# Optimization experiments

Measured on AMD Instinct MI355X. Metric: run time of the kernel, lower is better.

## Reference

```python
import jax, jax.numpy as jnp
import numpy as np

N_SRC = 50000
N_DST = 50000
N_EDGE = 600000
HID = 128
NUM_R = 6  # num_ratings + 1 weight matrices


def setup_inputs() -> dict:
    key = jax.random.key(0)
    ks = jax.random.split(key, 8)
    return {
        "src_features": jax.random.normal(ks[0], (N_SRC, HID), dtype=jnp.float32),
        "dst_features": jax.random.normal(ks[1], (N_DST, HID), dtype=jnp.float32),
        "W_r": jax.random.normal(ks[2], (NUM_R, HID, HID), dtype=jnp.float32),
        "W_lin": jax.random.normal(ks[3], (HID, 2 * HID), dtype=jnp.float32) / np.sqrt(2.0 * HID),
        "b_lin": jax.random.normal(ks[4], (HID,), dtype=jnp.float32) * 0.01,
        "edge_src": jax.random.randint(ks[5], (N_EDGE,), 0, N_SRC, dtype=jnp.int32),
        "edge_dst": jax.random.randint(ks[6], (N_EDGE,), 0, N_DST, dtype=jnp.int32),
        "rating": jax.random.randint(ks[7], (N_EDGE,), 0, NUM_R, dtype=jnp.int32),
    }


def reference(src_features, dst_features, W_r, W_lin, b_lin, edge_src, edge_dst, rating):
    # Gather source features per edge: [E, H]
    h_src = src_features[edge_src]
    # Per-edge rating-indexed matvec m_e = W_r[rating_e] @ h_src_e.
    # Avoid materializing [E, H, H] gathered weights: loop over the small
    # fixed set of rating matrices and mask-accumulate dense GEMMs.
    num_r = W_r.shape[0]
    m = jnp.zeros_like(h_src)
    for r in range(num_r):
        m = m + jnp.where((rating == r)[:, None], h_src @ W_r[r].T, jnp.zeros((), h_src.dtype))
    # Mean aggregation into destination nodes (0 for isolated nodes, like DGL).
    num_dst = dst_features.shape[0]
    sums = jax.ops.segment_sum(m, edge_dst, num_segments=num_dst)
    counts = jax.ops.segment_sum(jnp.ones((m.shape[0],), m.dtype), edge_dst, num_segments=num_dst)
    h_neigh = sums / jnp.maximum(counts, 1.0)[:, None]
    # concat + linear + relu
    h_cat = jnp.concatenate([dst_features, h_neigh], axis=1)  # [N_dst, 2H]
    return jax.nn.relu(h_cat @ W_lin.T + b_lin)
```

## Files before the change

### kernel.cpp

```cpp
#include <hip/hip_runtime.h>

#define HID 128
#define BM 128
#define BN 128
#define BKS 32
#define ALD 36
#define SCAN_BLK 256
#define SCAN_ELEMS 1024

typedef float v4f __attribute__((ext_vector_type(4)));
typedef short v4s __attribute__((ext_vector_type(4)));
typedef short v8s __attribute__((ext_vector_type(8)));

__device__ __forceinline__ void split_bf16(float v, unsigned short& hi, unsigned short& lo) {
  const unsigned int u = __float_as_uint(v);
  hi = (unsigned short)(u >> 16);
  const float rem = v - __uint_as_float(u & 0xffff0000u);
  lo = (unsigned short)(__float_as_uint(rem) >> 16);
}

__global__ void compose_Bt(const float* __restrict__ W_lin, const float* __restrict__ W_r,
                           unsigned short* __restrict__ Bth, unsigned short* __restrict__ Btl,
                           int KT) {
  const int k = blockIdx.x;
  const int n = threadIdx.x;
  float v;
  if (k < HID) {
    v = W_lin[n * (2 * HID) + k];
  } else {
    const int rr = (k - HID) >> 7;
    const int j  = (k - HID) & (HID - 1);
    const float* wl = W_lin + n * (2 * HID) + HID;
    const float* wr = W_r + (size_t)rr * HID * HID + j;
    float acc = 0.f;
#pragma unroll 8
    for (int i2 = 0; i2 < HID; ++i2)
      acc = fmaf(wl[i2], wr[i2 * HID], acc);
    v = acc;
  }
  unsigned short hi, lo;
  split_bf16(v, hi, lo);
  Bth[(size_t)n * KT + k] = hi;
  Btl[(size_t)n * KT + k] = lo;
}

__global__ void hist_kernel(const int* __restrict__ ed, const int* __restrict__ er,
                            int* __restrict__ hist, int NE, int NUMR) {
  const int i = blockIdx.x * blockDim.x + threadIdx.x;
  if (i < NE) atomicAdd(hist + ed[i] * NUMR + er[i], 1);
}

__global__ __launch_bounds__(SCAN_BLK)
void scan_phaseA(const int* __restrict__ cnt, int* __restrict__ partials, int n) {
  __shared__ int red[SCAN_BLK];
  const int tid = threadIdx.x;
  const int base = blockIdx.x * SCAN_ELEMS + tid * 4;
  int s = 0;
#pragma unroll
  for (int j = 0; j < 4; ++j) {
    const int i = base + j;
    if (i < n) s += cnt[i];
  }
  red[tid] = s;
  __syncthreads();
  for (int off = SCAN_BLK / 2; off > 0; off >>= 1) {
    if (tid < off) red[tid] += red[tid + off];
    __syncthreads();
  }
  if (tid == 0) partials[blockIdx.x] = red[0];
}

__global__ __launch_bounds__(1024)
void scan_phaseB(int* __restrict__ partials, int* __restrict__ offs_n, int nb) {
  __shared__ int ps[1024];
  const int tid = threadIdx.x;
  const int chunk = (nb + 1023) / 1024;
  const int b0 = tid * chunk;
  const int e0 = min(b0 + chunk, nb);
  int s = 0;
  for (int i = b0; i < e0; ++i) s += partials[i];
  ps[tid] = s;
  __syncthreads();
  for (int off = 1; off < 1024; off <<= 1) {
    const int t = (tid >= off) ? ps[tid - off] : 0;
    __syncthreads();
    ps[tid] += t;
    __syncthreads();
  }
  int run = ps[tid] - s;
  for (int i = b0; i < e0; ++i) {
    const int c = partials[i];
    partials[i] = run;
    run += c;
  }
  if (tid == 1023) offs_n[0] = ps[1023];
}

__global__ __launch_bounds__(SCAN_BLK)
void scan_phaseC(const int* __restrict__ cnt, const int* __restrict__ partials,
                 int* __restrict__ offs, int* __restrict__ cursor, int n) {
  __shared__ int tsum[SCAN_BLK];
  const int tid = threadIdx.x;
  const int base = blockIdx.x * SCAN_ELEMS + tid * 4;
  int v[4];
  int s = 0;
#pragma unroll
  for (int j = 0; j < 4; ++j) {
    const int i = base + j;
    v[j] = (i < n) ? cnt[i] : 0;
    s += v[j];
  }
  tsum[tid] = s;
  __syncthreads();
  for (int off = 1; off < SCAN_BLK; off <<= 1) {
    const int t = (tid >= off) ? tsum[tid - off] : 0;
    __syncthreads();
    tsum[tid] += t;
    __syncthreads();
  }
  int run = partials[blockIdx.x] + tsum[tid] - s;
#pragma unroll
  for (int j = 0; j < 4; ++j) {
    const int i = base + j;
    if (i < n) {
      offs[i] = run;
      cursor[i] = run;
      run += v[j];
    }
  }
}

__global__ void reorder_kernel(const int* __restrict__ es, const int* __restrict__ ed,
                               const int* __restrict__ er, int* __restrict__ cursor,
                               int* __restrict__ sorted, int NE, int NUMR) {
  const int i = blockIdx.x * blockDim.x + threadIdx.x;
  if (i < NE) {
    const int key = ed[i] * NUMR + er[i];
    const int pos = atomicAdd(cursor + key, 1);
    sorted[pos] = es[i];
  }
}

template <int NR>
__global__ __launch_bounds__(256)
void aggregate_dst(const float* __restrict__ src, const int* __restrict__ sorted,
                   const int* __restrict__ offs, float* __restrict__ S, int NDST) {
  const int d = (blockIdx.x * (blockDim.x >> 6)) + (threadIdx.x >> 6);
  if (d >= NDST) return;
  const int lane = threadIdx.x & 63;
  const int half = lane >> 5;
  const int c4 = (lane & 31) * 4;

  const int base = d * NR;
  const int o0 = offs[base];
  const int oN = offs[base + NR];
  int bnd[NR - 1];
#pragma unroll
  for (int r = 0; r < NR - 1; ++r) bnd[r] = offs[base + 1 + r];
  const float inv = 1.0f / fmaxf((float)(oN - o0), 1.0f);

  v4f a[NR];
#pragma unroll
  for (int r = 0; r < NR; ++r) a[r] = (v4f){0.f, 0.f, 0.f, 0.f};

  for (int e = o0 + half; e < oN; e += 2) {
    const int s = sorted[e];
    const v4f v = *reinterpret_cast<const v4f*>(src + (size_t)s * HID + c4);
    int rloc = 0;
#pragma unroll
    for (int r = 0; r < NR - 1; ++r) rloc += (e >= bnd[r]) ? 1 : 0;
#pragma unroll
    for (int r = 0; r < NR; ++r) {
      if (rloc == r) a[r] += v;
    }
  }

#pragma unroll
  for (int r = 0; r < NR; ++r) {
    v4f t = a[r];
    v4f o;
    o[0] = __shfl_xor(t[0], 32);
    o[1] = __shfl_xor(t[1], 32);
    o[2] = __shfl_xor(t[2], 32);
    o[3] = __shfl_xor(t[3], 32);
    t += o;
    if (half == 0) {
      t *= inv;
      __builtin_nontemporal_store(t,
          reinterpret_cast<v4f*>(S + (size_t)d * (NR * HID) + r * HID + c4));
    }
  }
}

__global__ __launch_bounds__(256)
void aggregate_kernel(const float* __restrict__ src, const int* __restrict__ sorted,
                      const int* __restrict__ offs, float* __restrict__ S,
                      int NDST, int NUMR) {
  const int wid = (blockIdx.x * (blockDim.x >> 6)) + (threadIdx.x >> 6);
  const int lane = threadIdx.x & 63;
  if (wid >= NDST * NUMR) return;
  const int d = wid / NUMR;
  const int rloc = wid - d * NUMR;
  const int k = d * NUMR + rloc;
  const int o0 = offs[k], o1 = offs[k + 1];
  const int c0 = offs[d * NUMR], c1 = offs[d * NUMR + NUMR];
  const float inv = 1.0f / fmaxf((float)(c1 - c0), 1.0f);
  float ax = 0.f, ay = 0.f;
  for (int e = o0; e < o1; ++e) {
    const int s = sorted[e];
    const float2 v = *reinterpret_cast<const float2*>(src + (size_t)s * HID + lane * 2);
    ax += v.x; ay += v.y;
  }
  *reinterpret_cast<float2*>(S + (size_t)d * (NUMR * HID) + rloc * HID + lane * 2) =
      make_float2(ax * inv, ay * inv);
}

__global__ __launch_bounds__(512)
void mfma_gemm(const float* __restrict__ dstf, const float* __restrict__ S,
               const unsigned short* __restrict__ Bth, const unsigned short* __restrict__ Btl,
               const float* __restrict__ b_lin, float* __restrict__ out,
               int M, int KT) {
  __shared__ unsigned short Ah[2][BM][ALD], Al[2][BM][ALD];
  __shared__ unsigned short Bh[2][BN][ALD], Bl[2][BN][ALD];

  const int tid = threadIdx.x;
  const int lane = tid & 63;
  const int wid = tid >> 6;
  const int wm = wid >> 1;
  const int wn = wid & 1;
  const int m0 = blockIdx.x * BM;
  const int l15 = lane & 15;
  const int kq = (lane >> 4) * 8;

  const int arow = tid >> 2;
  const int ac8 = (tid & 3) * 8;
  const int argr = m0 + arow;
  const int SSTRIDE = KT - HID;
  const int nkt = KT / BKS;

  v4f acc[2][4];
#pragma unroll
  for (int i = 0; i < 2; ++i)
#pragma unroll
    for (int j = 0; j < 4; ++j) acc[i][j] = (v4f){0.f, 0.f, 0.f, 0.f};

  float aReg[8];
  v8s bhReg, blReg;

  auto loadTile = [&](int kg) {
    v4f v0 = (v4f){0.f, 0.f, 0.f, 0.f};
    v4f v1 = (v4f){0.f, 0.f, 0.f, 0.f};
    if (argr < M) {
      const float* p = (kg < HID)
          ? dstf + (size_t)argr * HID + kg + ac8
          : S + (size_t)argr * SSTRIDE + (kg - HID) + ac8;
      v0 = __builtin_nontemporal_load(reinterpret_cast<const v4f*>(p));
      v1 = __builtin_nontemporal_load(reinterpret_cast<const v4f*>(p + 4));
    }
    aReg[0] = v0[0]; aReg[1] = v0[1]; aReg[2] = v0[2]; aReg[3] = v0[3];
    aReg[4] = v1[0]; aReg[5] = v1[1]; aReg[6] = v1[2]; aReg[7] = v1[3];
    const size_t gb = (size_t)arow * KT + kg + ac8;
    bhReg = *reinterpret_cast<const v8s*>(Bth + gb);
    blReg = *reinterpret_cast<const v8s*>(Btl + gb);
  };

  auto writeTile = [&](int p) {
    union { v4s v[2]; unsigned short u[8]; } hh, ll;
#pragma unroll
    for (int j = 0; j < 8; ++j) split_bf16(aReg[j], hh.u[j], ll.u[j]);
    *reinterpret_cast<v4s*>(&Ah[p][arow][ac8])     = hh.v[0];
    *reinterpret_cast<v4s*>(&Ah[p][arow][ac8 + 4]) = hh.v[1];
    *reinterpret_cast<v4s*>(&Al[p][arow][ac8])     = ll.v[0];
    *reinterpret_cast<v4s*>(&Al[p][arow][ac8 + 4]) = ll.v[1];
    union { v8s v; v4s h[2]; } bu;
    bu.v = bhReg;
    *reinterpret_cast<v4s*>(&Bh[p][arow][ac8])     = bu.h[0];
    *reinterpret_cast<v4s*>(&Bh[p][arow][ac8 + 4]) = bu.h[1];
    bu.v = blReg;
    *reinterpret_cast<v4s*>(&Bl[p][arow][ac8])     = bu.h[0];
    *reinterpret_cast<v4s*>(&Bl[p][arow][ac8 + 4]) = bu.h[1];
  };

  loadTile(0);
  writeTile(0);
  __syncthreads();

  int p = 0;
  for (int kt = 0; kt < nkt; ++kt) {
    const bool hasNext = (kt + 1) < nkt;
    if (hasNext) loadTile((kt + 1) * BKS);

    union { v8s v; v4s h[2]; } afh[2], afl[2], bfh[4], bfl[4];
#pragma unroll
    for (int fm = 0; fm < 2; ++fm) {
      const int r = wm * 32 + fm * 16 + l15;
      afh[fm].h[0] = *reinterpret_cast<const v4s*>(&Ah[p][r][kq]);
      afh[fm].h[1] = *reinterpret_cast<const v4s*>(&Ah[p][r][kq + 4]);
      afl[fm].h[0] = *reinterpret_cast<const v4s*>(&Al[p][r][kq]);
      afl[fm].h[1] = *reinterpret_cast<const v4s*>(&Al[p][r][kq + 4]);
    }
#pragma unroll
    for (int fn = 0; fn < 4; ++fn) {
      const int c = wn * 64 + fn * 16 + l15;
      bfh[fn].h[0] = *reinterpret_cast<const v4s*>(&Bh[p][c][kq]);
      bfh[fn].h[1] = *reinterpret_cast<const v4s*>(&Bh[p][c][kq + 4]);
      bfl[fn].h[0] = *reinterpret_cast<const v4s*>(&Bl[p][c][kq]);
      bfl[fn].h[1] = *reinterpret_cast<const v4s*>(&Bl[p][c][kq + 4]);
    }
#pragma unroll
    for (int fm = 0; fm < 2; ++fm)
#pragma unroll
      for (int fn = 0; fn < 4; ++fn) {
        acc[fm][fn] = __builtin_amdgcn_mfma_f32_16x16x32_bf16(afh[fm].v, bfh[fn].v, acc[fm][fn], 0, 0, 0);
        acc[fm][fn] = __builtin_amdgcn_mfma_f32_16x16x32_bf16(afh[fm].v, bfl[fn].v, acc[fm][fn], 0, 0, 0);
        acc[fm][fn] = __builtin_amdgcn_mfma_f32_16x16x32_bf16(afl[fm].v, bfh[fn].v, acc[fm][fn], 0, 0, 0);
      }

    if (hasNext) writeTile(p ^ 1);
    __syncthreads();
    p ^= 1;
  }

#pragma unroll
  for (int fn = 0; fn < 4; ++fn) {
    const int cn = wn * 64 + fn * 16 + l15;
    const float bias = b_lin[cn];
#pragma unroll
    for (int fm = 0; fm < 2; ++fm) {
      const int row0 = m0 + wm * 32 + fm * 16 + (lane >> 4) * 4;
#pragma unroll
      for (int r = 0; r < 4; ++r) {
        const int rg = row0 + r;
        if (rg < M) out[(size_t)rg * HID + cn] = fmaxf(acc[fm][fn][r] + bias, 0.f);
      }
    }
  }
}

extern "C" void kernel_launch(void* const* d_in, const int* in_sizes, int n_in,
                              void* d_out, int out_size, void* d_ws, size_t ws_size,
                              hipStream_t stream) {
  const float* src   = (const float*)d_in[0];
  const float* dstf  = (const float*)d_in[1];
  const float* W_r   = (const float*)d_in[2];
  const float* W_lin = (const float*)d_in[3];
  const float* b_lin = (const float*)d_in[4];
  const int* e_src   = (const int*)d_in[5];
  const int* e_dst   = (const int*)d_in[6];
  const int* e_rat   = (const int*)d_in[7];

  const int N_DST = in_sizes[1] / HID;
  const int NUM_R = in_sizes[2] / (HID * HID);
  const int NE = in_sizes[5];
  const int KT = HID + NUM_R * HID;
  const int NKEY = N_DST * NUM_R;
  const int NB = (NKEY + SCAN_ELEMS - 1) / SCAN_ELEMS;

  const size_t S_b      = (size_t)N_DST * (NUM_R * HID) * sizeof(float);
  const size_t hist_b   = (size_t)NKEY * sizeof(int);
  const size_t offs_b   = (size_t)(NKEY + 1) * sizeof(int);
  const size_t cursor_b = (size_t)NKEY * sizeof(int);
  const size_t sorted_b = (size_t)NE * sizeof(int);
  const size_t part_b   = (size_t)NB * sizeof(int);
  const size_t Bt_b     = (size_t)HID * KT * sizeof(unsigned short);
  const size_t need = S_b + hist_b + offs_b + cursor_b + sorted_b + part_b + 2 * Bt_b + 4096;
  if (ws_size < need) return;

  char* p = (char*)d_ws;
  float* S = (float*)p;            p += (S_b + 255) & ~(size_t)255;
  int* hist = (int*)p;             p += (hist_b + 255) & ~(size_t)255;
  int* offs = (int*)p;             p += (offs_b + 255) & ~(size_t)255;
  int* cursor = (int*)p;           p += (cursor_b + 255) & ~(size_t)255;
  int* sorted = (int*)p;           p += (sorted_b + 255) & ~(size_t)255;
  int* partials = (int*)p;         p += (part_b + 255) & ~(size_t)255;
  unsigned short* Bth = (unsigned short*)p;  p += (Bt_b + 255) & ~(size_t)255;
  unsigned short* Btl = (unsigned short*)p;

  compose_Bt<<<KT, HID, 0, stream>>>(W_lin, W_r, Bth, Btl, KT);
  hipMemsetAsync(hist, 0, hist_b, stream);
  hist_kernel<<<(NE + 255) / 256, 256, 0, stream>>>(e_dst, e_rat, hist, NE, NUM_R);
  scan_phaseA<<<NB, SCAN_BLK, 0, stream>>>(hist, partials, NKEY);
  scan_phaseB<<<1, 1024, 0, stream>>>(partials, offs + NKEY, NB);
  scan_phaseC<<<NB, SCAN_BLK, 0, stream>>>(hist, partials, offs, cursor, NKEY);
  reorder_kernel<<<(NE + 255) / 256, 256, 0, stream>>>(e_src, e_dst, e_rat, cursor,
                                                       sorted, NE, NUM_R);
  if (NUM_R == 6) {
    aggregate_dst<6><<<(N_DST + 3) / 4, 256, 0, stream>>>(src, sorted, offs, S, N_DST);
  } else {
    const int nwaves = N_DST * NUM_R;
    aggregate_kernel<<<(nwaves + 3) / 4, 256, 0, stream>>>(src, sorted, offs, S,
                                                           N_DST, NUM_R);
  }
  const int mb = (N_DST + BM - 1) / BM;
  mfma_gemm<<<mb, 512, 0, stream>>>(dstf, S, Bth, Btl, b_lin, (float*)d_out,
                                    N_DST, KT);
}
```

Before: 300.5 us.

## Deepen GEMM global prefetch to two stages and widen aggregation edge parallelism

The aggregation kernel now has each wavefront process four edges at once, with 16 lanes per edge and 8 floats per lane, then reduces across quarters with two shuffle steps. The goal is more independent gather loads in flight. The GEMM keeps two register staging buffers so global loads run two K-tiles ahead of the MFMA phase, with the loop unrolled by two over fixed LDS buffers. This hides more global latency but uses more registers, which may lower occupancy, and the aggregation keeps more accumulators live.

```diff
diff --git a/kernel.cpp b/kernel.cpp
--- a/kernel.cpp
+++ b/kernel.cpp
@@ -148,8 +148,8 @@
   const int d = (blockIdx.x * (blockDim.x >> 6)) + (threadIdx.x >> 6);
   if (d >= NDST) return;
   const int lane = threadIdx.x & 63;
-  const int half = lane >> 5;
-  const int c4 = (lane & 31) * 4;
+  const int q = lane >> 4;
+  const int c8 = (lane & 15) * 8;
 
   const int base = d * NR;
   const int o0 = offs[base];
@@ -159,35 +159,43 @@
   for (int r = 0; r < NR - 1; ++r) bnd[r] = offs[base + 1 + r];
   const float inv = 1.0f / fmaxf((float)(oN - o0), 1.0f);
 
-  v4f a[NR];
-#pragma unroll
-  for (int r = 0; r < NR; ++r) a[r] = (v4f){0.f, 0.f, 0.f, 0.f};
-
-  for (int e = o0 + half; e < oN; e += 2) {
+  v4f a0[NR], a1[NR];
+#pragma unroll
+  for (int r = 0; r < NR; ++r) {
+    a0[r] = (v4f){0.f, 0.f, 0.f, 0.f};
+    a1[r] = (v4f){0.f, 0.f, 0.f, 0.f};
+  }
+
+  for (int e = o0 + q; e < oN; e += 4) {
     const int s = sorted[e];
-    const v4f v = *reinterpret_cast<const v4f*>(src + (size_t)s * HID + c4);
+    const float* sp = src + (size_t)s * HID + c8;
+    const v4f v0 = *reinterpret_cast<const v4f*>(sp);
+    const v4f v1 = *reinterpret_cast<const v4f*>(sp + 4);
     int rloc = 0;
 #pragma unroll
     for (int r = 0; r < NR - 1; ++r) rloc += (e >= bnd[r]) ? 1 : 0;
 #pragma unroll
     for (int r = 0; r < NR; ++r) {
-      if (rloc == r) a[r] += v;
+      if (rloc == r) { a0[r] += v0; a1[r] += v1; }
     }
   }
 
 #pragma unroll
   for (int r = 0; r < NR; ++r) {
-    v4f t = a[r];
-    v4f o;
-    o[0] = __shfl_xor(t[0], 32);
-    o[1] = __shfl_xor(t[1], 32);
-    o[2] = __shfl_xor(t[2], 32);
-    o[3] = __shfl_xor(t[3], 32);
-    t += o;
-    if (half == 0) {
-      t *= inv;
-      __builtin_nontemporal_store(t,
-          reinterpret_cast<v4f*>(S + (size_t)d * (NR * HID) + r * HID + c4));
+    v4f t0 = a0[r], t1 = a1[r];
+#pragma unroll
+    for (int j = 0; j < 4; ++j) {
+      t0[j] += __shfl_xor(t0[j], 16);
+      t1[j] += __shfl_xor(t1[j], 16);
+      t0[j] += __shfl_xor(t0[j], 32);
+      t1[j] += __shfl_xor(t1[j], 32);
+    }
+    if (lane < 16) {
+      t0 *= inv;
+      t1 *= inv;
+      float* op = S + (size_t)d * (NR * HID) + r * HID + c8;
+      __builtin_nontemporal_store(t0, reinterpret_cast<v4f*>(op));
+      __builtin_nontemporal_store(t1, reinterpret_cast<v4f*>(op + 4));
     }
   }
 }
@@ -215,6 +223,8 @@
       make_float2(ax * inv, ay * inv);
 }
 
+struct Stage { v4f a0, a1; v8s bh, bl; };
+
 __global__ __launch_bounds__(512)
 void mfma_gemm(const float* __restrict__ dstf, const float* __restrict__ S,
                const unsigned short* __restrict__ Bth, const unsigned short* __restrict__ Btl,
@@ -244,52 +254,41 @@
 #pragma unroll
     for (int j = 0; j < 4; ++j) acc[i][j] = (v4f){0.f, 0.f, 0.f, 0.f};
 
-  float aReg[8];
-  v8s bhReg, blReg;
-
-  auto loadTile = [&](int kg) {
-    v4f v0 = (v4f){0.f, 0.f, 0.f, 0.f};
-    v4f v1 = (v4f){0.f, 0.f, 0.f, 0.f};
+  auto loadTile = [&](int kg, Stage& st) {
+    st.a0 = (v4f){0.f, 0.f, 0.f, 0.f};
+    st.a1 = (v4f){0.f, 0.f, 0.f, 0.f};
     if (argr < M) {
       const float* p = (kg < HID)
           ? dstf + (size_t)argr * HID + kg + ac8
           : S + (size_t)argr * SSTRIDE + (kg - HID) + ac8;
-      v0 = __builtin_nontemporal_load(reinterpret_cast<const v4f*>(p));
-      v1 = __builtin_nontemporal_load(reinterpret_cast<const v4f*>(p + 4));
-    }
-    aReg[0] = v0[0]; aReg[1] = v0[1]; aReg[2] = v0[2]; aReg[3] = v0[3];
-    aReg[4] = v1[0]; aReg[5] = v1[1]; aReg[6] = v1[2]; aReg[7] = v1[3];
+      st.a0 = __builtin_nontemporal_load(reinterpret_cast<const v4f*>(p));
+      st.a1 = __builtin_nontemporal_load(reinterpret_cast<const v4f*>(p + 4));
+    }
     const size_t gb = (size_t)arow * KT + kg + ac8;
-    bhReg = *reinterpret_cast<const v8s*>(Bth + gb);
-    blReg = *reinterpret_cast<const v8s*>(Btl + gb);
+    st.bh = *reinterpret_cast<const v8s*>(Bth + gb);
+    st.bl = *reinterpret_cast<const v8s*>(Btl + gb);
   };
 
-  auto writeTile = [&](int p) {
+  auto writeTile = [&](const Stage& st, int p) {
     union { v4s v[2]; unsigned short u[8]; } hh, ll;
 #pragma unroll
-    for (int j = 0; j < 8; ++j) split_bf16(aReg[j], hh.u[j], ll.u[j]);
+    for (int j = 0; j < 4; ++j) split_bf16(st.a0[j], hh.u[j], ll.u[j]);
+#pragma unroll
+    for (int j = 0; j < 4; ++j) split_bf16(st.a1[j], hh.u[4 + j], ll.u[4 + j]);
     *reinterpret_cast<v4s*>(&Ah[p][arow][ac8])     = hh.v[0];
     *reinterpret_cast<v4s*>(&Ah[p][arow][ac8 + 4]) = hh.v[1];
     *reinterpret_cast<v4s*>(&Al[p][arow][ac8])     = ll.v[0];
     *reinterpret_cast<v4s*>(&Al[p][arow][ac8 + 4]) = ll.v[1];
     union { v8s v; v4s h[2]; } bu;
-    bu.v = bhReg;
+    bu.v = st.bh;
     *reinterpret_cast<v4s*>(&Bh[p][arow][ac8])     = bu.h[0];
     *reinterpret_cast<v4s*>(&Bh[p][arow][ac8 + 4]) = bu.h[1];
-    bu.v = blReg;
+    bu.v = st.bl;
     *reinterpret_cast<v4s*>(&Bl[p][arow][ac8])     = bu.h[0];
     *reinterpret_cast<v4s*>(&Bl[p][arow][ac8 + 4]) = bu.h[1];
   };
 
-  loadTile(0);
-  writeTile(0);
-  __syncthreads();
-
-  int p = 0;
-  for (int kt = 0; kt < nkt; ++kt) {
-    const bool hasNext = (kt + 1) < nkt;
-    if (hasNext) loadTile((kt + 1) * BKS);
-
+  auto mfmaPhase = [&](int p) {
     union { v8s v; v4s h[2]; } afh[2], afl[2], bfh[4], bfl[4];
 #pragma unroll
     for (int fm = 0; fm < 2; ++fm) {
@@ -315,10 +314,24 @@
         acc[fm][fn] = __builtin_amdgcn_mfma_f32_16x16x32_bf16(afh[fm].v, bfl[fn].v, acc[fm][fn], 0, 0, 0);
         acc[fm][fn] = __builtin_amdgcn_mfma_f32_16x16x32_bf16(afl[fm].v, bfh[fn].v, acc[fm][fn], 0, 0, 0);
       }
-
-    if (hasNext) writeTile(p ^ 1);
-    __syncthreads();
-    p ^= 1;
+  };
+
+  Stage SA, SB;
+  loadTile(0, SA);
+  writeTile(SA, 0);
+  loadTile(BKS, SB);
+  __syncthreads();
+
+  for (int kt = 0; kt < nkt; kt += 2) {
+    if (kt + 2 < nkt) loadTile((kt + 2) * BKS, SA);
+    mfmaPhase(0);
+    if (kt + 1 < nkt) writeTile(SB, 1);
+    __syncthreads();
+    if (kt + 1 >= nkt) break;
+    if (kt + 3 < nkt) loadTile((kt + 3) * BKS, SB);
+    mfmaPhase(1);
+    if (kt + 2 < nkt) writeTile(SA, 0);
+    __syncthreads();
   }
 
 #pragma unroll
```

Result: slower. 336.2 us (+11.9%).
